# Performance work log

Measured on AMD Instinct MI355X. Metric: run time of the kernel, lower is better.

The kernel has to match this reference:

```python
import jax, jax.numpy as jnp
import numpy as np

B, D, E, H, A = 4096, 1024, 8, 1024, 512  # batch, state_dim, num_options, num_neurons, num_actions


def setup_inputs() -> dict:
    key = jax.random.key(0)
    ks = jax.random.split(key, 16)
    s = 0.02
    return {
        "state": jax.random.normal(ks[0], (B, D), jnp.float32),
        "selected_options": jax.random.randint(ks[1], (B,), 0, E, jnp.int32),
        # option network: Linear(D,H) -> ReLU -> Linear(H,E)
        "Wo1": jax.random.normal(ks[2], (D, H), jnp.float32) * s,
        "bo1": jnp.zeros((H,), jnp.float32),
        "Wo2": jax.random.normal(ks[3], (H, E), jnp.float32) * s,
        "bo2": jnp.zeros((E,), jnp.float32),
        # E expert nets, each: Linear(D,H)+ReLU -> Linear(H,H)+ReLU -> Linear(H,A)
        "We1": jax.random.normal(ks[4], (E, D, H), jnp.float32) * s,
        "be1": jnp.zeros((E, H), jnp.float32),
        "We2": jax.random.normal(ks[5], (E, H, H), jnp.float32) * s,
        "be2": jnp.zeros((E, H), jnp.float32),
        "We3": jax.random.normal(ks[6], (E, H, A), jnp.float32) * s,
        "be3": jnp.zeros((E, A), jnp.float32),
        # termination network: Linear(D,H) -> ReLU -> Linear(H,1) -> Sigmoid
        "Wt1": jax.random.normal(ks[7], (D, H), jnp.float32) * s,
        "bt1": jnp.zeros((H,), jnp.float32),
        "Wt2": jax.random.normal(ks[8], (H, 1), jnp.float32) * s,
        "bt2": jnp.zeros((1,), jnp.float32),
    }


def reference(state, selected_options, Wo1, bo1, Wo2, bo2,
              We1, be1, We2, be2, We3, be3, Wt1, bt1, Wt2, bt2):
    # option head
    option_probs = jax.nn.softmax(jnp.maximum(state @ Wo1 + bo1, 0.0) @ Wo2 + bo2, axis=-1)

    # expert MLPs: compute all experts vectorized, then gather per-sample selected expert.
    # (the torch code loops per sample; equal action sizes so no padding is needed)
    h = jnp.maximum(jnp.einsum("bd,edh->beh", state, We1) + be1, 0.0)   # [B,E,H]
    h = jnp.maximum(jnp.einsum("beh,ehk->bek", h, We2) + be2, 0.0)      # [B,E,H]
    logits = jnp.einsum("beh,eha->bea", h, We3) + be3                   # [B,E,A]
    probs_all = jax.nn.softmax(logits, axis=-1)
    sel = selected_options[:, None, None]
    action_probs = jnp.take_along_axis(probs_all, sel, axis=1)[:, 0, :]  # [B,A]
    selected_actions = jnp.argmax(action_probs, axis=-1)

    # termination head
    termination_prob = jax.nn.sigmoid(jnp.maximum(state @ Wt1 + bt1, 0.0) @ Wt2 + bt2)

    return option_probs, action_probs, termination_prob, selected_options, selected_actions
```

## Files before the change

### kernel.cpp

```cpp
#include <hip/hip_runtime.h>
#include <hip/hip_bf16.h>

#define B_ 4096
#define D_ 1024
#define E_ 8
#define H_ 1024
#define A_ 512
#define PB 6144
#define NTT 24
#define FB_CAP 128
#define FROWS (E_ * FB_CAP)
#define KSPLIT 4
#define MARGIN 3.0e-3f

typedef __attribute__((ext_vector_type(8))) short s16x8;
typedef __attribute__((ext_vector_type(4))) float f32x4;

__device__ __forceinline__ unsigned short f2bf(float f) {
    __hip_bfloat16 h = __float2bfloat16(f);
    return *reinterpret_cast<unsigned short*>(&h);
}
__device__ __forceinline__ float bf2f(unsigned short u) {
    return __uint_as_float(((unsigned int)u) << 16);
}
__device__ __forceinline__ void gload16(const void* g, void* l) {
    __builtin_amdgcn_global_load_lds(
        (const __attribute__((address_space(1))) unsigned int*)g,
        (__attribute__((address_space(3))) unsigned int*)l, 16, 0, 0);
}

__device__ __forceinline__ int a_src_chunk(int lane) { return (((lane & 7) ^ (lane >> 3)) * 8); }

__device__ __forceinline__ int trc(int r, int c) { return (c + r + (r >> 2)) & 63; }

__device__ __forceinline__ void tr_tile_256(const float* __restrict__ src, int Nsrc,
                                            unsigned short* __restrict__ dst, float* T) {
    const int t = threadIdx.x;
    const int c4 = (t & 15) * 4, r0 = t >> 4;
#pragma unroll
    for (int i = 0; i < 8; ++i) {
        const int r = r0 + i * 16;
        const float4 v = *(const float4*)&src[(size_t)r * Nsrc + c4];
        float* Tr = T + r * 64;
        Tr[trc(r, c4 + 0)] = v.x; Tr[trc(r, c4 + 1)] = v.y;
        Tr[trc(r, c4 + 2)] = v.z; Tr[trc(r, c4 + 3)] = v.w;
    }
    __syncthreads();
    const int k4 = (t & 31) * 4, n0 = t >> 5;
#pragma unroll
    for (int i = 0; i < 8; ++i) {
        const int n = n0 + i * 8;
        ushort4 o;
        o.x = f2bf(T[(k4 + 0) * 64 + trc(k4 + 0, n)]);
        o.y = f2bf(T[(k4 + 1) * 64 + trc(k4 + 1, n)]);
        o.z = f2bf(T[(k4 + 2) * 64 + trc(k4 + 2, n)]);
        o.w = f2bf(T[(k4 + 3) * 64 + trc(k4 + 3, n)]);
        *(ushort4*)&dst[(size_t)n * 1024 + k4] = o;
    }
}

__device__ __forceinline__ void tr_tile_512(const float* __restrict__ src, int Nsrc,
                                            unsigned short* __restrict__ dst, float* T) {
    const int t = threadIdx.x;
    const int c4 = (t & 15) * 4, r0 = t >> 4;
#pragma unroll
    for (int i = 0; i < 8; ++i) {
        const int r = r0 + i * 32;
        const float4 v = *(const float4*)&src[(size_t)r * Nsrc + c4];
        float* Tr = T + r * 64;
        Tr[trc(r, c4 + 0)] = v.x; Tr[trc(r, c4 + 1)] = v.y;
        Tr[trc(r, c4 + 2)] = v.z; Tr[trc(r, c4 + 3)] = v.w;
    }
    __syncthreads();
    const int k4 = (t & 63) * 4, n0 = t >> 6;
#pragma unroll
    for (int i = 0; i < 8; ++i) {
        const int n = n0 + i * 8;
        ushort4 o;
        o.x = f2bf(T[(k4 + 0) * 64 + trc(k4 + 0, n)]);
        o.y = f2bf(T[(k4 + 1) * 64 + trc(k4 + 1, n)]);
        o.z = f2bf(T[(k4 + 2) * 64 + trc(k4 + 2, n)]);
        o.w = f2bf(T[(k4 + 3) * 64 + trc(k4 + 3, n)]);
        *(ushort4*)&dst[(size_t)n * 1024 + k4] = o;
    }
}

__global__ void k_prep(const float* __restrict__ x, unsigned short* __restrict__ y,
                       const float* __restrict__ Wo1, const float* __restrict__ Wt1,
                       unsigned short* __restrict__ Wbf,
                       const float* __restrict__ We1, unsigned short* __restrict__ We1t,
                       const int* __restrict__ sel, int* __restrict__ tile_expert,
                       int* __restrict__ rowlist, int* __restrict__ pos_of_row,
                       int* __restrict__ rowlist2, int* __restrict__ cur2) {
    __shared__ float T[128 * 64];
    const int t = threadIdx.x;
    const int bid = blockIdx.x;
    if (bid >= 4353) {
        const int q = bid - 4353;
        const int e = q >> 7, r = q & 127, kt = r >> 4, ntb = r & 15;
        tr_tile_256(We1 + (size_t)e * 1048576 + (size_t)(kt * 128) * 1024 + ntb * 64, 1024,
                    We1t + (size_t)e * 1048576 + (size_t)(ntb * 64) * 1024 + kt * 128, T);
        return;
    }
    if (bid >= 4097) {
        const int q = bid - 4097;
        const int m = q >> 7, r = q & 127, kt = r >> 4, ntb = r & 15;
        const float* src = (m ? Wt1 : Wo1) + (size_t)(kt * 128) * 1024 + ntb * 64;
        tr_tile_256(src, 1024, Wbf + (size_t)(m * 1024 + ntb * 64) * 1024 + kt * 128, T);
        return;
    }
    if (bid > 0) {
        int i = (bid - 1) * 256 + t;
        float4 v = ((const float4*)x)[i];
        ushort4 o;
        o.x = f2bf(v.x); o.y = f2bf(v.y); o.z = f2bf(v.z); o.w = f2bf(v.w);
        ((ushort4*)y)[i] = o;
        return;
    }
    __shared__ int scnt[E_], soff[E_], scur[E_];
    if (t < E_) { scnt[t] = 0; scur[t] = 0; cur2[t] = 0; }
    for (int i = t; i < PB; i += 256) rowlist[i] = -1;
    for (int i = t; i < FROWS; i += 256) rowlist2[i] = -1;
    __syncthreads();
    for (int b = t; b < B_; b += 256) {
        int e = sel[b]; e = e < 0 ? 0 : (e >= E_ ? E_ - 1 : e);
        atomicAdd(&scnt[e], 1);
    }
    __syncthreads();
    if (t == 0) {
        int off = 0;
        for (int e = 0; e < E_; ++e) {
            soff[e] = off;
            int tiles = (scnt[e] + 255) >> 8;
            for (int k = 0; k < tiles; ++k) tile_expert[(off >> 8) + k] = e;
            off += tiles << 8;
        }
        for (int k = off >> 8; k < NTT; ++k) tile_expert[k] = -1;
    }
    __syncthreads();
    for (int b = t; b < B_; b += 256) {
        int e = sel[b]; e = e < 0 ? 0 : (e >= E_ ? E_ - 1 : e);
        int pos = atomicAdd(&scur[e], 1);
        int p = soff[e] + pos; if (p >= PB) p = PB - 1;
        rowlist[p] = b;
        pos_of_row[b] = p;
    }
}

template<int TN>
__device__ __forceinline__ void gemm3(
    const unsigned short* __restrict__ g0, const unsigned short* __restrict__ g1,
    const unsigned short* __restrict__ g2, const unsigned short* __restrict__ g3,
    const unsigned short* __restrict__ Bt, int Kg, const float* __restrict__ bp,
    unsigned short* __restrict__ Cbf, float* __restrict__ Cf, int Ncols, int relu,
    unsigned short* As, unsigned short* Bs)
{
    constexpr int NI = TN / 32;
    constexpr int BTH = TN * 64;
    constexpr int BR = TN / 64;
    const int t = threadIdx.x, lane = t & 63, w = t >> 6;
    const int wr = w >> 1, wc = w & 1;
    const int aseg = w * 2048 + lane * 8;
    const int bseg = w * (BR * 512) + lane * 8;
    const int coffb = a_src_chunk(lane);
    const unsigned short* bsrc = Bt + (size_t)(w * BR * 8 + (lane >> 3)) * Kg + coffb;

    f32x4 acc[4][NI];
#pragma unroll
    for (int i = 0; i < 4; ++i)
#pragma unroll
        for (int j = 0; j < NI; ++j)
#pragma unroll
            for (int r = 0; r < 4; ++r) acc[i][j][r] = 0.f;

#define G_STAGE(IT, BUF) {                                                   \
        const int ko_ = (IT) * 64;                                           \
        const int oa_ = (BUF) * 16384 + aseg;                                \
        gload16(g0 + ko_, As + oa_);                                         \
        gload16(g1 + ko_, As + oa_ + 512);                                   \
        gload16(g2 + ko_, As + oa_ + 1024);                                  \
        gload16(g3 + ko_, As + oa_ + 1536);                                  \
        const int ob_ = (BUF) * BTH + bseg;                                  \
        _Pragma("unroll")                                                    \
        for (int j_ = 0; j_ < BR; ++j_)                                      \
            gload16(bsrc + ko_ + (size_t)(j_ * 8) * Kg, Bs + ob_ + j_ * 512); \
    }

    G_STAGE(0, 0);
    __syncthreads();

    for (int it = 0; it < 16; ++it) {
        const int cb = it & 1;
        if (it + 1 < 16) G_STAGE(it + 1, cb ^ 1);
        __builtin_amdgcn_s_setprio(1);
#pragma unroll
        for (int kq = 0; kq < 2; ++kq) {
            const int sc = kq * 4 + (lane >> 4);
            s16x8 af[4], bfr[NI];
#pragma unroll
            for (int mi = 0; mi < 4; ++mi) {
                const int ar = wr * 64 + mi * 16 + (lane & 15);
                af[mi] = *reinterpret_cast<const s16x8*>(
                    &As[cb * 16384 + ar * 64 + ((sc ^ (ar & 7)) << 3)]);
            }
#pragma unroll
            for (int ni = 0; ni < NI; ++ni) {
                const int br = wc * (TN / 2) + ni * 16 + (lane & 15);
                bfr[ni] = *reinterpret_cast<const s16x8*>(
                    &Bs[cb * BTH + br * 64 + ((sc ^ (br & 7)) << 3)]);
            }
#pragma unroll
            for (int mi = 0; mi < 4; ++mi)
#pragma unroll
                for (int ni = 0; ni < NI; ++ni)
                    acc[mi][ni] = __builtin_amdgcn_mfma_f32_16x16x32_bf16(
                        af[mi], bfr[ni], acc[mi][ni], 0, 0, 0);
        }
        __builtin_amdgcn_s_setprio(0);
        if (it + 1 < 16) __syncthreads();
    }
#undef G_STAGE

    const int cq = lane >> 4, cr = lane & 15;
#pragma unroll
    for (int ni = 0; ni < NI; ++ni) {
        const int col_l = wc * (TN / 2) + ni * 16 + cr;
        const float bv = bp[col_l];
#pragma unroll
        for (int mi = 0; mi < 4; ++mi) {
#pragma unroll
            for (int r = 0; r < 4; ++r) {
                const int row_l = wr * 64 + mi * 16 + cq * 4 + r;
                float v = acc[mi][ni][r] + bv;
                if (relu) v = fmaxf(v, 0.f);
                const size_t idx = (size_t)row_l * Ncols + col_l;
                if (Cbf) Cbf[idx] = f2bf(v);
                if (Cf)  Cf[idx] = v;
            }
        }
    }
}

__global__ __launch_bounds__(512, 2)
void k_d2(const unsigned short* __restrict__ Sbf,
          const int* __restrict__ rowlist, const int* __restrict__ tile_expert,
          const unsigned short* __restrict__ Wbf,
          const float* __restrict__ bo1, const float* __restrict__ bt1,
          const unsigned short* __restrict__ We1t, const float* __restrict__ be1,
          const float* __restrict__ We2, unsigned short* __restrict__ We2t,
          unsigned short* __restrict__ hopt, unsigned short* __restrict__ hterm,
          unsigned short* __restrict__ h1) {
    __shared__ __align__(16) unsigned short SMEM[4 * 16384];
    unsigned short* As = SMEM;
    unsigned short* Bs = SMEM + 2 * 16384;
    const int bid = blockIdx.x;
    if (bid >= 224) {
        const int q = bid - 224;
        const int e = q >> 6, r = q & 63, kt = r >> 4, ntb = r & 15;
        tr_tile_512(We2 + (size_t)e * 1048576 + (size_t)(kt * 256) * 1024 + ntb * 64, 1024,
                    We2t + (size_t)e * 1048576 + (size_t)(ntb * 64) * 1024 + kt * 256,
                    (float*)SMEM);
        return;
    }
    const int t = threadIdx.x, lane = t & 63, w = t >> 6;
    const int coff = a_src_chunk(lane);
    const int r0l = w * 32 + (lane >> 3);
    if (bid < 128) {
        const int nt = bid & 7, mt = bid >> 3;
        const unsigned short* g0 = Sbf + (size_t)(mt * 256 + r0l) * D_ + coff;
        const unsigned short* g1 = g0 + (size_t)8 * D_;
        const unsigned short* g2 = g0 + (size_t)16 * D_;
        const unsigned short* g3 = g0 + (size_t)24 * D_;
        int ntRow; const float* bp; unsigned short* C;
        if (nt < 4) { ntRow = nt * 256; bp = bo1 + nt * 256;
                      C = hopt + (size_t)(mt * 256) * H_ + nt * 256; }
        else { ntRow = 1024 + (nt - 4) * 256; bp = bt1 + (nt - 4) * 256;
               C = hterm + (size_t)(mt * 256) * H_ + (nt - 4) * 256; }
        gemm3<256>(g0, g1, g2, g3, Wbf + (size_t)ntRow * 1024, 1024, bp,
                   C, nullptr, H_, 1, As, Bs);
    } else {
        const int q = bid - 128, nt = q & 3, mt = q >> 2;
        const int e = tile_expert[mt]; if (e < 0) return;
        const int base = mt * 256;
        const int sub = rowlist[base]; if (sub < 0) return;
        int r0 = rowlist[base + r0l];      if (r0 < 0) r0 = sub;
        int r1 = rowlist[base + r0l + 8];  if (r1 < 0) r1 = sub;
        int r2 = rowlist[base + r0l + 16]; if (r2 < 0) r2 = sub;
        int r3 = rowlist[base + r0l + 24]; if (r3 < 0) r3 = sub;
        const unsigned short* g0 = Sbf + (size_t)r0 * D_ + coff;
        const unsigned short* g1 = Sbf + (size_t)r1 * D_ + coff;
        const unsigned short* g2 = Sbf + (size_t)r2 * D_ + coff;
        const unsigned short* g3 = Sbf + (size_t)r3 * D_ + coff;
        gemm3<256>(g0, g1, g2, g3,
                   We1t + (size_t)e * 1048576 + (size_t)(nt * 256) * 1024, 1024,
                   be1 + (size_t)e * H_ + nt * 256,
                   h1 + (size_t)(mt * 256) * H_ + nt * 256, nullptr, H_, 1, As, Bs);
    }
}

__global__ __launch_bounds__(512, 2)
void k_d3(const unsigned short* __restrict__ h1, const int* __restrict__ tile_expert,
          const unsigned short* __restrict__ We2t, const float* __restrict__ be2,
          const float* __restrict__ We3, unsigned short* __restrict__ We3t,
          unsigned short* __restrict__ h2) {
    __shared__ __align__(16) unsigned short SMEM[2 * 16384 + 2 * 8192];
    unsigned short* As = SMEM;
    unsigned short* Bs = SMEM + 2 * 16384;
    const int bid = blockIdx.x;
    if (bid >= 192) {
        const int q = bid - 192;
        const int e = q >> 5, r = q & 31, kt = r >> 3, ntb = r & 7;
        tr_tile_512(We3 + (size_t)e * 524288 + (size_t)(kt * 256) * 512 + ntb * 64, 512,
                    We3t + (size_t)e * 524288 + (size_t)(ntb * 64) * 1024 + kt * 256,
                    (float*)SMEM);
        return;
    }
    const int t = threadIdx.x, lane = t & 63, w = t >> 6;
    const int coff = a_src_chunk(lane);
    const int r0l = w * 32 + (lane >> 3);
    const int nt = bid & 7, mt = bid >> 3;
    const int e = tile_expert[mt]; if (e < 0) return;
    const unsigned short* g0 = h1 + (size_t)(mt * 256 + r0l) * H_ + coff;
    gemm3<128>(g0, g0 + (size_t)8 * H_, g0 + (size_t)16 * H_, g0 + (size_t)24 * H_,
               We2t + (size_t)e * 1048576 + (size_t)(nt * 128) * 1024, 1024,
               be2 + (size_t)e * H_ + nt * 128,
               h2 + (size_t)(mt * 256) * H_ + nt * 128, nullptr, H_, 1, As, Bs);
}

__global__ __launch_bounds__(512, 2)
void k_d5(const unsigned short* __restrict__ h2, const int* __restrict__ tile_expert,
          const unsigned short* __restrict__ We3t, const float* __restrict__ be3,
          float* __restrict__ lgt) {
    __shared__ __align__(16) unsigned short SMEM[2 * 16384 + 2 * 4096];
    unsigned short* As = SMEM;
    unsigned short* Bs = SMEM + 2 * 16384;
    const int t = threadIdx.x, lane = t & 63, w = t >> 6;
    const int coff = a_src_chunk(lane);
    const int r0l = w * 32 + (lane >> 3);
    const int nt = blockIdx.x & 7, mt = blockIdx.x >> 3;
    const int e = tile_expert[mt]; if (e < 0) return;
    const unsigned short* g0 = h2 + (size_t)(mt * 256 + r0l) * H_ + coff;
    gemm3<64>(g0, g0 + (size_t)8 * H_, g0 + (size_t)16 * H_, g0 + (size_t)24 * H_,
              We3t + (size_t)e * 524288 + (size_t)(nt * 64) * 1024, 1024,
              be3 + (size_t)e * A_ + nt * 64,
              nullptr, lgt + (size_t)(mt * 256) * A_ + nt * 64, A_, 0, As, Bs);
}

__device__ __forceinline__ void opt_body(int b, const unsigned short* __restrict__ h,
                                         const float* __restrict__ Wo2, const float* __restrict__ bo2,
                                         float* __restrict__ out, float* sm) {
    const int t = threadIdx.x;
    float acc[E_];
#pragma unroll
    for (int j = 0; j < E_; ++j) acc[j] = 0.f;
    for (int k = t; k < H_; k += 256) {
        float hv = bf2f(h[(size_t)b * H_ + k]);
#pragma unroll
        for (int j = 0; j < E_; ++j) acc[j] = fmaf(hv, Wo2[k * E_ + j], acc[j]);
    }
#pragma unroll
    for (int j = 0; j < E_; ++j)
        for (int off = 32; off; off >>= 1) acc[j] += __shfl_down(acc[j], off, 64);
    float* red = sm;
    float* probs = sm + 4 * E_;
    int wave = t >> 6, lane = t & 63;
    if (lane == 0)
        for (int j = 0; j < E_; ++j) red[wave * E_ + j] = acc[j];
    __syncthreads();
    if (t == 0) {
        float z[E_]; float m = -1e30f;
        for (int j = 0; j < E_; ++j) {
            z[j] = red[j] + red[E_ + j] + red[2 * E_ + j] + red[3 * E_ + j] + bo2[j];
            m = fmaxf(m, z[j]);
        }
        float s = 0.f;
        for (int j = 0; j < E_; ++j) { z[j] = expf(z[j] - m); s += z[j]; }
        float inv = 1.f / s;
        for (int j = 0; j < E_; ++j) probs[j] = z[j] * inv;
    }
    __syncthreads();
    if (t < E_) out[(size_t)b * E_ + t] = probs[t];
}

__device__ __forceinline__ void term_body(int b, const unsigned short* __restrict__ h,
                                          const float* __restrict__ Wt2, const float* __restrict__ bt2,
                                          float* __restrict__ out, float* sm) {
    const int t = threadIdx.x;
    float acc = 0.f;
    for (int k = t; k < H_; k += 256) acc = fmaf(bf2f(h[(size_t)b * H_ + k]), Wt2[k], acc);
    for (int off = 32; off; off >>= 1) acc += __shfl_down(acc, off, 64);
    if ((t & 63) == 0) sm[t >> 6] = acc;
    __syncthreads();
    if (t == 0) {
        float z = sm[0] + sm[1] + sm[2] + sm[3] + bt2[0];
        out[b] = 1.f / (1.f + expf(-z));
    }
}

__global__ __launch_bounds__(256)
void k_gather(const float* __restrict__ logits, const int* __restrict__ pos_of_row,
              const int* __restrict__ sel,
              float* __restrict__ out_probs, float* __restrict__ out_selopt,
              float* __restrict__ out_selact,
              int* __restrict__ rowlist2, int* __restrict__ cur2,
              const unsigned short* __restrict__ hopt, const float* __restrict__ Wo2,
              const float* __restrict__ bo2, float* __restrict__ out_opt,
              const unsigned short* __restrict__ hterm, const float* __restrict__ Wt2,
              const float* __restrict__ bt2, float* __restrict__ out_term) {
    __shared__ float smbuf[5 * E_ + 8];
    const int bid = blockIdx.x;
    if (bid >= 2 * B_) { term_body(bid - 2 * B_, hterm, Wt2, bt2, out_term, smbuf); return; }
    if (bid >= B_)     { opt_body(bid - B_, hopt, Wo2, bo2, out_opt, smbuf); return; }

    const int b = bid;
    int p = pos_of_row[b];
    if (p < 0) p = 0; if (p >= PB) p = PB - 1;
    const int t = threadIdx.x;
    const float* L = logits + (size_t)p * A_;
    float v0 = L[t], v1 = L[t + 256];

    float bv; int bi;
    if (v0 >= v1) { bv = v0; bi = t; } else { bv = v1; bi = t + 256; }
    for (int off = 32; off; off >>= 1) {
        float ov = __shfl_down(bv, off, 64);
        int   oi = __shfl_down(bi, off, 64);
        if (ov > bv || (ov == bv && oi < bi)) { bv = ov; bi = oi; }
    }
    __shared__ float rv[4]; __shared__ int ri[4];
    int wave = t >> 6, lane = t & 63;
    if (lane == 0) { rv[wave] = bv; ri[wave] = bi; }
    __syncthreads();
    __shared__ float sM; __shared__ int sBi;
    if (t == 0) {
        float mv = rv[0]; int mi = ri[0];
        for (int w = 1; w < 4; ++w)
            if (rv[w] > mv || (rv[w] == mv && ri[w] < mi)) { mv = rv[w]; mi = ri[w]; }
        sM = mv; sBi = mi;
    }
    __syncthreads();
    const float M = sM; const int BI = sBi;

    float e0 = expf(v0 - M), e1 = expf(v1 - M);
    float s = e0 + e1;
    for (int off = 32; off; off >>= 1) s += __shfl_down(s, off, 64);
    __shared__ float reds[4];
    if (lane == 0) reds[wave] = s;
    __syncthreads();
    float inv = 1.f / (reds[0] + reds[1] + reds[2] + reds[3]);

    out_probs[(size_t)b * A_ + t]       = e0 * inv;
    out_probs[(size_t)b * A_ + t + 256] = e1 * inv;

    float s0 = (t == BI) ? -1e30f : v0;
    float s1 = (t + 256 == BI) ? -1e30f : v1;
    float sm = fmaxf(s0, s1);
    for (int off = 32; off; off >>= 1) sm = fmaxf(sm, __shfl_down(sm, off, 64));
    __shared__ float red2[4];
    if (lane == 0) red2[wave] = sm;
    __syncthreads();

    if (t == 0) {
        float second = fmaxf(fmaxf(red2[0], red2[1]), fmaxf(red2[2], red2[3]));
        out_selact[b] = (float)BI;
        int e = sel[b]; e = e < 0 ? 0 : (e >= E_ ? E_ - 1 : e);
        out_selopt[b] = (float)sel[b];
        if (M - second < MARGIN) {
            int pos = atomicAdd(&cur2[e], 1);
            if (pos < FB_CAP) rowlist2[e * FB_CAP + pos] = b;
        }
    }
}

#define BM 64
#define BN 64
#define BK 32

__global__ __launch_bounds__(256)
void k_pgemm(const float* __restrict__ A, int lda, const int* __restrict__ flags,
             int gather, const float* __restrict__ W,
             float* __restrict__ P, int K, int N) {
    __shared__ float As_[BK][BM + 4];
    __shared__ float Bs_[BK][BN];

    const int mt = blockIdx.y, nt = blockIdx.x, kz = blockIdx.z;
    if (flags[mt * BM] < 0) return;
    const int e = mt >> 1;
    const float* Wb = W + (size_t)e * K * N + (size_t)nt * BN;

    const int t  = threadIdx.x;
    const int tx = t & 15;
    const int ty = t >> 4;

    const int arow = t >> 3;
    const int ak   = (t & 7) * 4;
    int r0 = mt * BM + arow, r1 = r0 + 32;
    if (gather) { r0 = flags[r0]; r1 = flags[r1]; }
    const int bkr = t >> 4;
    const int bn  = (t & 15) * 4;

    float acc[4][4];
#pragma unroll
    for (int i = 0; i < 4; ++i)
#pragma unroll
        for (int j = 0; j < 4; ++j) acc[i][j] = 0.0f;

    const int kbeg = kz * (K / KSPLIT);
    const int kend = kbeg + (K / KSPLIT);
    for (int k0 = kbeg; k0 < kend; k0 += BK) {
        float4 a0 = make_float4(0.f, 0.f, 0.f, 0.f), a1 = a0;
        if (r0 >= 0) a0 = *(const float4*)&A[(size_t)r0 * lda + k0 + ak];
        if (r1 >= 0) a1 = *(const float4*)&A[(size_t)r1 * lda + k0 + ak];
        float4 b0 = *(const float4*)&Wb[(size_t)(k0 + bkr) * N + bn];
        float4 b1 = *(const float4*)&Wb[(size_t)(k0 + bkr + 16) * N + bn];

        __syncthreads();
        As_[ak + 0][arow] = a0.x; As_[ak + 1][arow] = a0.y;
        As_[ak + 2][arow] = a0.z; As_[ak + 3][arow] = a0.w;
        As_[ak + 0][arow + 32] = a1.x; As_[ak + 1][arow + 32] = a1.y;
        As_[ak + 2][arow + 32] = a1.z; As_[ak + 3][arow + 32] = a1.w;
        *(float4*)&Bs_[bkr][bn]      = b0;
        *(float4*)&Bs_[bkr + 16][bn] = b1;
        __syncthreads();

#pragma unroll
        for (int kk = 0; kk < BK; ++kk) {
            const float4 av = *(const float4*)&As_[kk][ty * 4];
            const float4 bv = *(const float4*)&Bs_[kk][tx * 4];
            const float a_[4] = {av.x, av.y, av.z, av.w};
            const float b_[4] = {bv.x, bv.y, bv.z, bv.w};
#pragma unroll
            for (int i = 0; i < 4; ++i)
#pragma unroll
                for (int j = 0; j < 4; ++j)
                    acc[i][j] = fmaf(a_[i], b_[j], acc[i][j]);
        }
    }

    float* Pz = P + (size_t)kz * FROWS * N;
    const int n0 = nt * BN + tx * 4;
#pragma unroll
    for (int i = 0; i < 4; ++i) {
        int m = mt * BM + ty * 4 + i;
        *(float4*)&Pz[(size_t)m * N + n0] = make_float4(acc[i][0], acc[i][1], acc[i][2], acc[i][3]);
    }
}

__global__ __launch_bounds__(256)
void k_fred(const float* __restrict__ P, const int* __restrict__ flags,
            const float* __restrict__ bias, float* __restrict__ C, int N, int relu) {
    const int m = blockIdx.x;
    if (flags[m] < 0) return;
    const int e = m >> 7;
    const int t = threadIdx.x;
    if (t * 4 >= N) return;
    const size_t MN = (size_t)FROWS * N;
    const size_t base = (size_t)m * N + t * 4;
    float4 s = *(const float4*)&P[base];
#pragma unroll
    for (int z = 1; z < KSPLIT; ++z) {
        float4 p = *(const float4*)&P[(size_t)z * MN + base];
        s.x += p.x; s.y += p.y; s.z += p.z; s.w += p.w;
    }
    const float* bp = bias + (size_t)e * N + t * 4;
    s.x += bp[0]; s.y += bp[1]; s.z += bp[2]; s.w += bp[3];
    if (relu) {
        s.x = fmaxf(s.x, 0.f); s.y = fmaxf(s.y, 0.f);
        s.z = fmaxf(s.z, 0.f); s.w = fmaxf(s.w, 0.f);
    }
    *(float4*)&C[base] = s;
}

__global__ __launch_bounds__(256)
void k_fixup(const float* __restrict__ logitsf, const int* __restrict__ rowlist2,
             float* __restrict__ out_probs, float* __restrict__ out_selact) {
    const int i = blockIdx.x;
    const int row = rowlist2[i];
    if (row < 0) return;
    const int t = threadIdx.x;
    const float* L = logitsf + (size_t)i * A_;
    float v0 = L[t], v1 = L[t + 256];

    float bv; int bi;
    if (v0 >= v1) { bv = v0; bi = t; } else { bv = v1; bi = t + 256; }
    for (int off = 32; off; off >>= 1) {
        float ov = __shfl_down(bv, off, 64);
        int   oi = __shfl_down(bi, off, 64);
        if (ov > bv || (ov == bv && oi < bi)) { bv = ov; bi = oi; }
    }
    __shared__ float rv[4]; __shared__ int ri[4];
    int wave = t >> 6, lane = t & 63;
    if (lane == 0) { rv[wave] = bv; ri[wave] = bi; }
    __syncthreads();
    __shared__ float sM; __shared__ int sBi;
    if (t == 0) {
        float mv = rv[0]; int mi = ri[0];
        for (int w = 1; w < 4; ++w)
            if (rv[w] > mv || (rv[w] == mv && ri[w] < mi)) { mv = rv[w]; mi = ri[w]; }
        sM = mv; sBi = mi;
    }
    __syncthreads();

    float e0 = expf(v0 - sM), e1 = expf(v1 - sM);
    float s = e0 + e1;
    for (int off = 32; off; off >>= 1) s += __shfl_down(s, off, 64);
    __shared__ float reds[4];
    if (lane == 0) reds[wave] = s;
    __syncthreads();
    float inv = 1.f / (reds[0] + reds[1] + reds[2] + reds[3]);

    out_probs[(size_t)row * A_ + t]       = e0 * inv;
    out_probs[(size_t)row * A_ + t + 256] = e1 * inv;
    if (t == 0) out_selact[row] = (float)sBi;
}

extern "C" void kernel_launch(void* const* d_in, const int* in_sizes, int n_in,
                              void* d_out, int out_size, void* d_ws, size_t ws_size,
                              hipStream_t stream) {
    const float* state = (const float*)d_in[0];
    const int*   sel   = (const int*)d_in[1];
    const float* Wo1 = (const float*)d_in[2];
    const float* bo1 = (const float*)d_in[3];
    const float* Wo2 = (const float*)d_in[4];
    const float* bo2 = (const float*)d_in[5];
    const float* We1 = (const float*)d_in[6];
    const float* be1 = (const float*)d_in[7];
    const float* We2 = (const float*)d_in[8];
    const float* be2 = (const float*)d_in[9];
    const float* We3 = (const float*)d_in[10];
    const float* be3 = (const float*)d_in[11];
    const float* Wt1 = (const float*)d_in[12];
    const float* bt1 = (const float*)d_in[13];
    const float* Wt2 = (const float*)d_in[14];
    const float* bt2 = (const float*)d_in[15];
    float* out = (float*)d_out;

    char* w = (char*)d_ws;
    int* meta        = (int*)w;
    int* rowlist     = meta;
    int* pos_of_row  = meta + 6144;
    int* rowlist2    = meta + 10240;
    int* tile_expert = meta + 11264;
    int* cur2        = meta + 11296;
    char* P0 = w + 65536;
    char* P1 = P0 + 12582912;
    char* P2 = P1 + 16777216;
    char* W1 = P2 + 12582912;
    char* W2 = W1 + 16777216;
    unsigned short* Sbf   = (unsigned short*)P0;
    unsigned short* Wbf   = (unsigned short*)(P0 + (8u << 20));
    unsigned short* h2b   = (unsigned short*)P0;
    unsigned short* hopt  = (unsigned short*)P1;
    unsigned short* hterm = hopt + (size_t)B_ * H_;
    unsigned short* h1b   = (unsigned short*)P2;
    unsigned short* We1t  = (unsigned short*)W1;
    unsigned short* We3t  = (unsigned short*)W1;
    unsigned short* We2t  = (unsigned short*)W2;
    float* lgt  = (float*)P2;
    float* Pbuf = (float*)P1;
    float* h1f  = (float*)P0;
    float* h2f  = h1f + (size_t)FROWS * H_;
    float* lgf  = h2f + (size_t)FROWS * H_;

    size_t act_off    = (size_t)B_ * E_;
    size_t term_off   = act_off + (size_t)B_ * A_;
    size_t selopt_off = term_off + B_;
    size_t selact_off = selopt_off + B_;

    k_prep<<<5377, 256, 0, stream>>>(state, Sbf, Wo1, Wt1, Wbf, We1, We1t,
                                     sel, tile_expert, rowlist, pos_of_row, rowlist2, cur2);

    k_d2<<<736, 512, 0, stream>>>(Sbf, rowlist, tile_expert, Wbf,
                                  bo1, bt1, We1t, be1, We2, We2t, hopt, hterm, h1b);
    k_d3<<<448, 512, 0, stream>>>(h1b, tile_expert, We2t, be2, We3, We3t, h2b);
    k_d5<<<192, 512, 0, stream>>>(h2b, tile_expert, We3t, be3, lgt);

    k_gather<<<3 * B_, 256, 0, stream>>>(lgt, pos_of_row, sel,
                                         out + act_off, out + selopt_off, out + selact_off,
                                         rowlist2, cur2,
                                         hopt, Wo2, bo2, out,
                                         hterm, Wt2, bt2, out + term_off);

    k_pgemm<<<dim3(H_ / BN, FROWS / BM, KSPLIT), 256, 0, stream>>>(state, D_, rowlist2, 1, We1, Pbuf, D_, H_);
    k_fred<<<FROWS, 256, 0, stream>>>(Pbuf, rowlist2, be1, h1f, H_, 1);
    k_pgemm<<<dim3(H_ / BN, FROWS / BM, KSPLIT), 256, 0, stream>>>(h1f, H_, rowlist2, 0, We2, Pbuf, H_, H_);
    k_fred<<<FROWS, 256, 0, stream>>>(Pbuf, rowlist2, be2, h2f, H_, 1);
    k_pgemm<<<dim3(A_ / BN, FROWS / BM, KSPLIT), 256, 0, stream>>>(h2f, H_, rowlist2, 0, We3, Pbuf, H_, A_);
    k_fred<<<FROWS, 256, 0, stream>>>(Pbuf, rowlist2, be3, lgf, A_, 0);
    k_fixup<<<FROWS, 256, 0, stream>>>(lgf, rowlist2, out + act_off, out + selact_off);
}
```

Before: 208.2 us.

## Move We2/We3 transposes into prep kernel, out of the GEMM launches

The bf16 transposes of We2 and We3 now run as extra blocks in k_prep using the 256-thread tile routine, instead of as trailing blocks inside the k_d2 and k_d3 GEMM launches. We3t gets its own workspace region instead of aliasing We1t, so it no longer has to wait for We1t to be consumed. This keeps the GEMM kernels uniform and removes the memory-bound tail blocks that compete with them. The cost is a larger prep launch and 16 MB more workspace.

```diff
diff --git a/kernel.cpp b/kernel.cpp
--- a/kernel.cpp
+++ b/kernel.cpp
@@ -59,42 +59,32 @@
     }
 }
 
-__device__ __forceinline__ void tr_tile_512(const float* __restrict__ src, int Nsrc,
-                                            unsigned short* __restrict__ dst, float* T) {
-    const int t = threadIdx.x;
-    const int c4 = (t & 15) * 4, r0 = t >> 4;
-#pragma unroll
-    for (int i = 0; i < 8; ++i) {
-        const int r = r0 + i * 32;
-        const float4 v = *(const float4*)&src[(size_t)r * Nsrc + c4];
-        float* Tr = T + r * 64;
-        Tr[trc(r, c4 + 0)] = v.x; Tr[trc(r, c4 + 1)] = v.y;
-        Tr[trc(r, c4 + 2)] = v.z; Tr[trc(r, c4 + 3)] = v.w;
-    }
-    __syncthreads();
-    const int k4 = (t & 63) * 4, n0 = t >> 6;
-#pragma unroll
-    for (int i = 0; i < 8; ++i) {
-        const int n = n0 + i * 8;
-        ushort4 o;
-        o.x = f2bf(T[(k4 + 0) * 64 + trc(k4 + 0, n)]);
-        o.y = f2bf(T[(k4 + 1) * 64 + trc(k4 + 1, n)]);
-        o.z = f2bf(T[(k4 + 2) * 64 + trc(k4 + 2, n)]);
-        o.w = f2bf(T[(k4 + 3) * 64 + trc(k4 + 3, n)]);
-        *(ushort4*)&dst[(size_t)n * 1024 + k4] = o;
-    }
-}
-
 __global__ void k_prep(const float* __restrict__ x, unsigned short* __restrict__ y,
                        const float* __restrict__ Wo1, const float* __restrict__ Wt1,
                        unsigned short* __restrict__ Wbf,
                        const float* __restrict__ We1, unsigned short* __restrict__ We1t,
+                       const float* __restrict__ We2, unsigned short* __restrict__ We2t,
+                       const float* __restrict__ We3, unsigned short* __restrict__ We3t,
                        const int* __restrict__ sel, int* __restrict__ tile_expert,
                        int* __restrict__ rowlist, int* __restrict__ pos_of_row,
                        int* __restrict__ rowlist2, int* __restrict__ cur2) {
     __shared__ float T[128 * 64];
     const int t = threadIdx.x;
     const int bid = blockIdx.x;
+    if (bid >= 6401) {
+        const int q = bid - 6401;
+        const int e = q >> 6, r = q & 63, kt = r >> 3, ntb = r & 7;
+        tr_tile_256(We3 + (size_t)e * 524288 + (size_t)(kt * 128) * 512 + ntb * 64, 512,
+                    We3t + (size_t)e * 524288 + (size_t)(ntb * 64) * 1024 + kt * 128, T);
+        return;
+    }
+    if (bid >= 5377) {
+        const int q = bid - 5377;
+        const int e = q >> 7, r = q & 127, kt = r >> 4, ntb = r & 15;
+        tr_tile_256(We2 + (size_t)e * 1048576 + (size_t)(kt * 128) * 1024 + ntb * 64, 1024,
+                    We2t + (size_t)e * 1048576 + (size_t)(ntb * 64) * 1024 + kt * 128, T);
+        return;
+    }
     if (bid >= 4353) {
         const int q = bid - 4353;
         const int e = q >> 7, r = q & 127, kt = r >> 4, ntb = r & 15;
@@ -247,21 +237,12 @@
           const unsigned short* __restrict__ Wbf,
           const float* __restrict__ bo1, const float* __restrict__ bt1,
           const unsigned short* __restrict__ We1t, const float* __restrict__ be1,
-          const float* __restrict__ We2, unsigned short* __restrict__ We2t,
           unsigned short* __restrict__ hopt, unsigned short* __restrict__ hterm,
           unsigned short* __restrict__ h1) {
     __shared__ __align__(16) unsigned short SMEM[4 * 16384];
     unsigned short* As = SMEM;
     unsigned short* Bs = SMEM + 2 * 16384;
     const int bid = blockIdx.x;
-    if (bid >= 224) {
-        const int q = bid - 224;
-        const int e = q >> 6, r = q & 63, kt = r >> 4, ntb = r & 15;
-        tr_tile_512(We2 + (size_t)e * 1048576 + (size_t)(kt * 256) * 1024 + ntb * 64, 1024,
-                    We2t + (size_t)e * 1048576 + (size_t)(ntb * 64) * 1024 + kt * 256,
-                    (float*)SMEM);
-        return;
-    }
     const int t = threadIdx.x, lane = t & 63, w = t >> 6;
     const int coff = a_src_chunk(lane);
     const int r0l = w * 32 + (lane >> 3);
@@ -301,24 +282,14 @@
 __global__ __launch_bounds__(512, 2)
 void k_d3(const unsigned short* __restrict__ h1, const int* __restrict__ tile_expert,
           const unsigned short* __restrict__ We2t, const float* __restrict__ be2,
-          const float* __restrict__ We3, unsigned short* __restrict__ We3t,
           unsigned short* __restrict__ h2) {
     __shared__ __align__(16) unsigned short SMEM[2 * 16384 + 2 * 8192];
     unsigned short* As = SMEM;
     unsigned short* Bs = SMEM + 2 * 16384;
-    const int bid = blockIdx.x;
-    if (bid >= 192) {
-        const int q = bid - 192;
-        const int e = q >> 5, r = q & 31, kt = r >> 3, ntb = r & 7;
-        tr_tile_512(We3 + (size_t)e * 524288 + (size_t)(kt * 256) * 512 + ntb * 64, 512,
-                    We3t + (size_t)e * 524288 + (size_t)(ntb * 64) * 1024 + kt * 256,
-                    (float*)SMEM);
-        return;
-    }
     const int t = threadIdx.x, lane = t & 63, w = t >> 6;
     const int coff = a_src_chunk(lane);
     const int r0l = w * 32 + (lane >> 3);
-    const int nt = bid & 7, mt = bid >> 3;
+    const int nt = blockIdx.x & 7, mt = blockIdx.x >> 3;
     const int e = tile_expert[mt]; if (e < 0) return;
     const unsigned short* g0 = h1 + (size_t)(mt * 256 + r0l) * H_ + coff;
     gemm3<128>(g0, g0 + (size_t)8 * H_, g0 + (size_t)16 * H_, g0 + (size_t)24 * H_,
@@ -646,6 +617,7 @@
     char* P2 = P1 + 16777216;
     char* W1 = P2 + 12582912;
     char* W2 = W1 + 16777216;
+    char* W3 = W2 + 16777216;
     unsigned short* Sbf   = (unsigned short*)P0;
     unsigned short* Wbf   = (unsigned short*)(P0 + (8u << 20));
     unsigned short* h2b   = (unsigned short*)P0;
@@ -653,8 +625,8 @@
     unsigned short* hterm = hopt + (size_t)B_ * H_;
     unsigned short* h1b   = (unsigned short*)P2;
     unsigned short* We1t  = (unsigned short*)W1;
-    unsigned short* We3t  = (unsigned short*)W1;
     unsigned short* We2t  = (unsigned short*)W2;
+    unsigned short* We3t  = (unsigned short*)W3;
     float* lgt  = (float*)P2;
     float* Pbuf = (float*)P1;
     float* h1f  = (float*)P0;
@@ -666,12 +638,13 @@
     size_t selopt_off = term_off + B_;
     size_t selact_off = selopt_off + B_;
 
-    k_prep<<<5377, 256, 0, stream>>>(state, Sbf, Wo1, Wt1, Wbf, We1, We1t,
+    k_prep<<<6913, 256, 0, stream>>>(state, Sbf, Wo1, Wt1, Wbf, We1, We1t,
+                                     We2, We2t, We3, We3t,
                                      sel, tile_expert, rowlist, pos_of_row, rowlist2, cur2);
 
-    k_d2<<<736, 512, 0, stream>>>(Sbf, rowlist, tile_expert, Wbf,
-                                  bo1, bt1, We1t, be1, We2, We2t, hopt, hterm, h1b);
-    k_d3<<<448, 512, 0, stream>>>(h1b, tile_expert, We2t, be2, We3, We3t, h2b);
+    k_d2<<<224, 512, 0, stream>>>(Sbf, rowlist, tile_expert, Wbf,
+                                  bo1, bt1, We1t, be1, hopt, hterm, h1b);
+    k_d3<<<192, 512, 0, stream>>>(h1b, tile_expert, We2t, be2, h2b);
     k_d5<<<192, 512, 0, stream>>>(h2b, tile_expert, We3t, be3, lgt);
 
     k_gather<<<3 * B_, 256, 0, stream>>>(lgt, pos_of_row, sel,
```

Result: no change. 211.4 us (+1.5%).
